# Optimization experiments

Hardware: AMD Instinct MI355X
Metric: run time of the kernel (lower is better)

The kernel has to match this reference:

```python
import jax, jax.numpy as jnp
import numpy as np

# Poincare ball hyperbolic multi-head attention (hypll-style HMultiheadAttention)
C = 1.0          # ball curvature
SQRT_C = 1.0
EPS = 1e-7
B, S, E, H = 4, 1024, 512, 8
HD = E // H      # head_dim = 64


def _project_to_ball(u, scale=0.5):
    n = jnp.linalg.norm(u, axis=-1, keepdims=True)
    return u * (scale / (1.0 + n))  # guarantees ||x|| < scale < 1/sqrt(C)


def h_linear(x, z, r):
    """Poincare fully-connected layer (Shimizu et al. HNN++), as in hypll HLinear.
    x: [..., n] points in the ball, z: [n, m] weight directions, r: [m] bias."""
    x2 = jnp.sum(x * x, -1, keepdims=True)
    lam = 2.0 / jnp.maximum(1.0 - C * x2, EPS)          # conformal factor lambda_x
    zn = jnp.maximum(jnp.linalg.norm(z, axis=0), EPS)    # [m]
    xz = x @ z                                           # [..., m]
    two_cr = 2.0 * SQRT_C * r
    v = (2.0 * zn / SQRT_C) * jnp.arcsinh(
        SQRT_C * lam * xz / zn * jnp.cosh(two_cr) - (lam - 1.0) * jnp.sinh(two_cr)
    )
    v2 = jnp.sum(v * v, -1, keepdims=True)
    return v / (1.0 + jnp.sqrt(1.0 + C * v2))            # map back into the ball


def _split_heads(x):
    b, s, e = x.shape
    return x.reshape(b, s, H, HD).transpose(0, 2, 1, 3)  # [B,H,S,hd]; matches split(dim=-1)


def _h_attention(q, k, v):
    # similarity = -poincare_dist(q, k), pairwise via the arccosh closed form
    # (avoids materializing a [B,H,Sq,Sk,hd] mobius_add tensor)
    q2 = jnp.sum(q * q, -1)[..., :, None]                # [B,H,Sq,1]
    k2 = jnp.sum(k * k, -1)[..., None, :]                # [B,H,1,Sk]
    qk = jnp.einsum('bhqd,bhkd->bhqk', q, k)
    diff2 = jnp.maximum(q2 + k2 - 2.0 * qk, 0.0)
    denom = jnp.maximum((1.0 - C * q2) * (1.0 - C * k2), EPS)
    arg = 1.0 + 2.0 * C * diff2 / denom
    dist = jnp.arccosh(jnp.maximum(arg, 1.0 + EPS)) / SQRT_C
    w = jax.nn.softmax(-dist, axis=-1)                   # attention_activation
    # attention_midpoint: weighted Mobius gyromidpoint then half scalar-mul
    v2 = jnp.sum(v * v, -1)                              # [B,H,Sk]
    lam = 2.0 / jnp.maximum(1.0 - C * v2, EPS)
    num = jnp.einsum('bhqk,bhkd->bhqd', w * lam[..., None, :], v)
    den = jnp.einsum('bhqk,bhk->bhq', w, lam - 1.0)[..., None]
    m_bar = num / jnp.where(jnp.abs(den) < EPS, EPS, den)
    mn = jnp.maximum(jnp.linalg.norm(m_bar, axis=-1, keepdims=True), EPS)
    t = jnp.minimum(SQRT_C * mn, 1.0 - 1e-6)
    return jnp.tanh(0.5 * jnp.arctanh(t)) * m_bar / (SQRT_C * mn)  # (1/2) mobius-scalar-mul


def setup_inputs() -> dict:
    key = jax.random.key(0)
    ks = jax.random.split(key, 9)
    query = _project_to_ball(jax.random.normal(ks[0], (B, S, E), jnp.float32))
    key_t = _project_to_ball(jax.random.normal(ks[1], (B, S, E), jnp.float32))
    value = _project_to_ball(jax.random.normal(ks[2], (B, S, E), jnp.float32))
    scale = E ** -0.5
    zq = jax.random.normal(ks[3], (E, E), jnp.float32) * scale
    zk = jax.random.normal(ks[4], (E, E), jnp.float32) * scale
    zv = jax.random.normal(ks[5], (E, E), jnp.float32) * scale
    rq = jax.random.normal(ks[6], (E,), jnp.float32) * 0.01
    rk = jax.random.normal(ks[7], (E,), jnp.float32) * 0.01
    rv = jax.random.normal(ks[8], (E,), jnp.float32) * 0.01
    return {"query": query, "key": key_t, "value": value,
            "zq": zq, "rq": rq, "zk": zk, "rk": rk, "zv": zv, "rv": rv}


def reference(query, key, value, zq, rq, zk, rk, zv, rv):
    pq = h_linear(query, zq, rq)
    pk = h_linear(key, zk, rk)
    pv = h_linear(value, zv, rv)
    q, k, v = _split_heads(pq), _split_heads(pk), _split_heads(pv)
    out = _h_attention(q, k, v)                          # [B,H,S,hd]
    return out.transpose(0, 2, 1, 3).reshape(B, S, E)    # manifold.cat over heads
```

## Files before the change

kernel.cpp:

```cpp
#include <hip/hip_runtime.h>
#include <hip/hip_bf16.h>
#include <math.h>

#define EPSf 1e-7f
typedef unsigned short u16;
typedef __attribute__((ext_vector_type(8))) short bf16x8;
typedef __attribute__((ext_vector_type(4))) float f32x4;

__device__ __forceinline__ float bf2f(u16 u) {
  union { unsigned int i; float f; } x; x.i = ((unsigned int)u) << 16; return x.f;
}
__device__ __forceinline__ u16 f2bf(float f) {
  union { float f; unsigned int i; } x; x.f = f;
  unsigned int r = x.i + 0x7fffu + ((x.i >> 16) & 1u);
  return (u16)(r >> 16);
}
__device__ __forceinline__ void gll16(const void* g, void* l) {
  __builtin_amdgcn_global_load_lds((__attribute__((address_space(1))) void*)(g),
                                   (__attribute__((address_space(3))) void*)(l),
                                   16, 0, 0);
}

__global__ __launch_bounds__(256) void split_x(
    const float* __restrict__ xq, const float* __restrict__ xk, const float* __restrict__ xv,
    u16* __restrict__ Xh, u16* __restrict__ Xl,
    float* __restrict__ Xn, float* __restrict__ Vn, float* __restrict__ Zn) {
  if (blockIdx.x == 0) {
    #pragma unroll
    for (int j = 0; j < 6; ++j) Zn[threadIdx.x + 256 * j] = 0.f;
  }
  const int gr = blockIdx.x * 2 + (threadIdx.x >> 7);
  const int mat = gr >> 12, row = gr & 4095;
  const float* X = (mat == 0) ? xq : (mat == 1) ? xk : xv;
  const int f4 = threadIdx.x & 127;
  float4 x = ((const float4*)(X + (size_t)row * 512))[f4];
  u16 h0 = f2bf(x.x), h1 = f2bf(x.y), h2 = f2bf(x.z), h3 = f2bf(x.w);
  u16 l0 = f2bf(x.x - bf2f(h0)), l1 = f2bf(x.y - bf2f(h1));
  u16 l2 = f2bf(x.z - bf2f(h2)), l3 = f2bf(x.w - bf2f(h3));
  ((ushort4*)(Xh + (size_t)gr * 512))[f4] = make_ushort4(h0, h1, h2, h3);
  ((ushort4*)(Xl + (size_t)gr * 512))[f4] = make_ushort4(l0, l1, l2, l3);
  float a = fmaf(x.x, x.x, fmaf(x.y, x.y, fmaf(x.z, x.z, x.w * x.w)));
  a += __shfl_xor(a, 1);  a += __shfl_xor(a, 2);  a += __shfl_xor(a, 4);
  a += __shfl_xor(a, 8);  a += __shfl_xor(a, 16); a += __shfl_xor(a, 32);
  __shared__ float red[4];
  if ((threadIdx.x & 63) == 0) red[threadIdx.x >> 6] = a;
  __syncthreads();
  if (threadIdx.x == 0)   { Xn[gr] = red[0] + red[1]; Vn[gr] = 0.f; }
  if (threadIdx.x == 128) { Xn[gr] = red[2] + red[3]; Vn[gr] = 0.f; }
}

__global__ __launch_bounds__(256) void split_z(
    const float* __restrict__ zq, const float* __restrict__ zk, const float* __restrict__ zv,
    u16* __restrict__ ZhT, u16* __restrict__ ZlT, float* __restrict__ Zn) {
  const int idx = blockIdx.x;
  const int mat = idx >> 6;
  const int cg = (idx >> 3) & 7, kt = idx & 7;
  const int c0 = cg * 64;
  const float* Z = (mat == 0) ? zq : (mat == 1) ? zk : zv;
  __shared__ float tile[64][68];
  const int t = threadIdx.x;
  {
    int kl = t >> 2;
    const float* src = Z + (size_t)(kt * 64 + kl) * 512 + c0 + (t & 3) * 16;
    #pragma unroll
    for (int j = 0; j < 4; ++j) {
      float4 v = *(const float4*)(src + 4 * j);
      *(float4*)&tile[kl][(t & 3) * 16 + 4 * j] = v;
    }
  }
  __syncthreads();
  const int cl = t >> 2, kg4 = t & 3;
  const size_t zo = (size_t)mat * 512 * 512;
  float csum = 0.f;
  #pragma unroll
  for (int jj = 0; jj < 4; ++jj) {
    u16 hb[4], lb[4];
    #pragma unroll
    for (int qq = 0; qq < 4; ++qq) {
      float zval = tile[kg4 * 16 + jj * 4 + qq][cl];
      csum = fmaf(zval, zval, csum);
      u16 hh = f2bf(zval);
      hb[qq] = hh;
      lb[qq] = f2bf(zval - bf2f(hh));
    }
    size_t o = zo + (size_t)(c0 + cl) * 512 + kt * 64 + kg4 * 16 + jj * 4;
    *(ushort4*)(ZhT + o) = make_ushort4(hb[0], hb[1], hb[2], hb[3]);
    *(ushort4*)(ZlT + o) = make_ushort4(lb[0], lb[1], lb[2], lb[3]);
  }
  csum += __shfl_xor(csum, 1);
  csum += __shfl_xor(csum, 2);
  if (kg4 == 0) atomicAdd(&Zn[mat * 512 + c0 + cl], csum);
}

__global__ __launch_bounds__(256) void proj_gemm(
    const u16* __restrict__ Xh, const u16* __restrict__ Xl,
    const u16* __restrict__ ZhT, const u16* __restrict__ ZlT,
    const float* __restrict__ Xn, const float* __restrict__ Zn,
    const float* __restrict__ rq, const float* __restrict__ rk, const float* __restrict__ rv,
    float* __restrict__ Vtmp, float* __restrict__ Vn) {
  const int m0 = blockIdx.x * 64;
  const int n0 = blockIdx.y * 128;
  const int mat = blockIdx.z;
  const size_t xoff = (size_t)mat * 4096 * 512;
  const size_t zoff = (size_t)mat * 512 * 512;
  const int t = threadIdx.x, wv = t >> 6, lane = t & 63;
  const int l15 = lane & 15, quad = lane >> 4;
  const int wm = wv >> 1, wn = wv & 1;

  __shared__ __align__(16) u16 SM[12288];
  __shared__ float lams[64], lam1s[64], wmxs[128], wmys[128], wmzs[128];

  if (t < 64) {
    float x2 = Xn[mat * 4096 + m0 + t];
    float lam = 2.f / fmaxf(1.f - x2, EPSf);
    lams[t] = lam; lam1s[t] = lam - 1.f;
  }
  if (t < 128) {
    float zn = fmaxf(sqrtf(Zn[mat * 512 + n0 + t]), EPSf);
    const float* R = (mat == 0) ? rq : (mat == 1) ? rk : rv;
    float tr = 2.f * R[n0 + t];
    float e = expf(tr), ei = 1.f / e;
    wmxs[t] = 0.5f * (e + ei) / zn;
    wmys[t] = 0.5f * (e - ei);
    wmzs[t] = 2.f * zn;
  }

  f32x4 acc[2][4];
  #pragma unroll
  for (int i = 0; i < 2; ++i)
    #pragma unroll
    for (int j = 0; j < 4; ++j) acc[i][j] = (f32x4){0.f, 0.f, 0.f, 0.f};

  const u16* gs[6];
  u16* ld[6];
  #pragma unroll
  for (int ci = 0; ci < 6; ++ci) {
    int c = wv + 4 * ci;
    const u16* arr; int row0, lo;
    if (c < 4)       { arr = Xh + xoff;  row0 = m0 + 16 * c;        lo = c * 512; }
    else if (c < 8)  { arr = Xl + xoff;  row0 = m0 + 16 * (c - 4);  lo = 2048 + (c - 4) * 512; }
    else if (c < 16) { arr = ZhT + zoff; row0 = n0 + 16 * (c - 8);  lo = 4096 + (c - 8) * 512; }
    else             { arr = ZlT + zoff; row0 = n0 + 16 * (c - 16); lo = 8192 + (c - 16) * 512; }
    gs[ci] = arr + (size_t)(row0 + (lane >> 2)) * 512 + (lane & 3) * 8;
    ld[ci] = SM + lo;
  }

  for (int k0 = 0; k0 < 512; k0 += 32) {
    __syncthreads();
    #pragma unroll
    for (int ci = 0; ci < 6; ++ci) gll16(gs[ci] + k0, ld[ci]);
    __syncthreads();
    bf16x8 ah[2], al[2], bh_[4], bl_[4];
    #pragma unroll
    for (int i = 0; i < 2; ++i) {
      int ra = wm * 32 + i * 16 + l15;
      ah[i] = *(const bf16x8*)&SM[ra * 32 + quad * 8];
      al[i] = *(const bf16x8*)&SM[2048 + ra * 32 + quad * 8];
    }
    #pragma unroll
    for (int j = 0; j < 4; ++j) {
      int rb = wn * 64 + j * 16 + l15;
      bh_[j] = *(const bf16x8*)&SM[4096 + rb * 32 + quad * 8];
      bl_[j] = *(const bf16x8*)&SM[8192 + rb * 32 + quad * 8];
    }
    #pragma unroll
    for (int i = 0; i < 2; ++i)
      #pragma unroll
      for (int j = 0; j < 4; ++j) {
        acc[i][j] = __builtin_amdgcn_mfma_f32_16x16x32_bf16(ah[i], bh_[j], acc[i][j], 0, 0, 0);
        acc[i][j] = __builtin_amdgcn_mfma_f32_16x16x32_bf16(ah[i], bl_[j], acc[i][j], 0, 0, 0);
        acc[i][j] = __builtin_amdgcn_mfma_f32_16x16x32_bf16(al[i], bh_[j], acc[i][j], 0, 0, 0);
      }
  }

  #pragma unroll
  for (int i = 0; i < 2; ++i) {
    float rsum[4] = {0.f, 0.f, 0.f, 0.f};
    #pragma unroll
    for (int j = 0; j < 4; ++j) {
      int nl = wn * 64 + j * 16 + l15;
      float wx = wmxs[nl], wy = wmys[nl], wz = wmzs[nl];
      #pragma unroll
      for (int r = 0; r < 4; ++r) {
        int ml = wm * 32 + i * 16 + quad * 4 + r;
        float tt = lams[ml] * acc[i][j][r] * wx - lam1s[ml] * wy;
        float v = wz * logf(tt + sqrtf(fmaf(tt, tt, 1.f)));
        Vtmp[xoff + (size_t)(m0 + ml) * 512 + (n0 + nl)] = v;
        rsum[r] = fmaf(v, v, rsum[r]);
      }
    }
    #pragma unroll
    for (int r = 0; r < 4; ++r) {
      rsum[r] += __shfl_xor(rsum[r], 1);
      rsum[r] += __shfl_xor(rsum[r], 2);
      rsum[r] += __shfl_xor(rsum[r], 4);
      rsum[r] += __shfl_xor(rsum[r], 8);
    }
    if (l15 == 0) {
      #pragma unroll
      for (int r = 0; r < 4; ++r)
        atomicAdd(&Vn[mat * 4096 + m0 + wm * 32 + i * 16 + quad * 4 + r], rsum[r]);
    }
  }
}

__global__ __launch_bounds__(256) void pack(
    const float* __restrict__ Vtmp, const float* __restrict__ Vn,
    u16* __restrict__ Qh, u16* __restrict__ Kh, u16* __restrict__ VTb,
    float* __restrict__ q2a, float* __restrict__ aqa, float4* __restrict__ ksc) {
  __shared__ u16 tile[64][72];
  __shared__ float lams[64];
  const int t = threadIdx.x;
  if (blockIdx.x < 256) {
    const int mat = blockIdx.x >> 7;
    const int rb = blockIdx.x & 127;
    const int r = t >> 3, h = t & 7;
    const int row = rb * 32 + r;
    const size_t gr = (size_t)mat * 4096 + row;
    const float sc = 1.f / (1.f + sqrtf(1.f + Vn[gr]));
    const float* src = Vtmp + gr * 512 + h * 64;
    const int b = row >> 10, s = row & 1023;
    u16* dst = (mat ? Kh : Qh) + ((size_t)(b * 8 + h) * 1024 + s) * 64;
    float nrm = 0.f;
    #pragma unroll
    for (int j = 0; j < 16; ++j) {
      float4 x = *(const float4*)(src + 4 * j);
      u16 u0 = f2bf(x.x * sc), u1 = f2bf(x.y * sc), u2 = f2bf(x.z * sc), u3 = f2bf(x.w * sc);
      *(ushort4*)(dst + 4 * j) = make_ushort4(u0, u1, u2, u3);
      float f0 = bf2f(u0), f1 = bf2f(u1), f2 = bf2f(u2), f3 = bf2f(u3);
      nrm += f0 * f0 + f1 * f1 + f2 * f2 + f3 * f3;
    }
    const size_t so = (size_t)(b * 8 + h) * 1024 + s;
    if (mat == 0) { q2a[so] = nrm; aqa[so] = 1.f / fmaxf(1.f - nrm, EPSf); }
    else {
      float2 kk = make_float2(nrm, 2.f / fmaxf(1.f - nrm, EPSf));
      *(float2*)&ksc[so] = kk;
    }
  } else {
    const int idx = blockIdx.x - 256;
    const int bh = idx >> 4, st = idx & 15;
    const int b = bh >> 3, h = bh & 7;
    {
      const int s = t >> 2, dg = t & 3;
      const size_t gr = (size_t)2 * 4096 + b * 1024 + st * 64 + s;
      const float sc = 1.f / (1.f + sqrtf(1.f + Vn[gr]));
      const float* src = Vtmp + gr * 512 + h * 64 + dg * 16;
      float nrm = 0.f;
      #pragma unroll
      for (int j = 0; j < 4; ++j) {
        float4 x = *(const float4*)(src + 4 * j);
        u16 u0 = f2bf(x.x * sc), u1 = f2bf(x.y * sc), u2 = f2bf(x.z * sc), u3 = f2bf(x.w * sc);
        *(ushort4*)&tile[s][dg * 16 + 4 * j] = make_ushort4(u0, u1, u2, u3);
        float f0 = bf2f(u0), f1 = bf2f(u1), f2 = bf2f(u2), f3 = bf2f(u3);
        nrm += f0 * f0 + f1 * f1 + f2 * f2 + f3 * f3;
      }
      nrm += __shfl_xor(nrm, 1);
      nrm += __shfl_xor(nrm, 2);
      if (dg == 0) {
        float lam = 2.f / fmaxf(1.f - nrm, EPSf);
        lams[s] = lam;
        ((float*)&ksc[(size_t)bh * 1024 + st * 64 + s])[3] = lam - 1.f;
      }
    }
    __syncthreads();
    const int d = t >> 2, sg = t & 3;
    u16 ob[16];
    #pragma unroll
    for (int j = 0; j < 16; ++j) {
      int ss = sg * 16 + j;
      ob[j] = f2bf(bf2f(tile[ss][d]) * lams[ss]);
    }
    u16* dst = VTb + ((size_t)bh * 64 + d) * 1024 + st * 64 + sg * 16;
    #pragma unroll
    for (int j = 0; j < 4; ++j)
      *(ushort4*)(dst + 4 * j) = make_ushort4(ob[4 * j], ob[4 * j + 1], ob[4 * j + 2], ob[4 * j + 3]);
  }
}

__global__ __launch_bounds__(256, 2) void attn(
    const u16* __restrict__ Qh, const u16* __restrict__ Kh, const u16* __restrict__ VTb,
    const float* __restrict__ q2a, const float* __restrict__ aqa,
    const float4* __restrict__ ksc, float* __restrict__ out) {
  const int bh = blockIdx.x;
  const int b = bh >> 3, h = bh & 7;
  const int q0 = blockIdx.y * 64;
  const int t = threadIdx.x, wv = t >> 6, lane = t & 63;
  const int l15 = lane & 15, quad = lane >> 4;
  const int qh = wv & 1, kh = wv >> 1;

  __shared__ __align__(16) u16 Ws[4][32 * 72];
  __shared__ float k2s[4][64], cks[4][64], l1s[4][64];
  __shared__ __align__(16) float nums[2][32][68];
  __shared__ float dens[2][32];

  const size_t qkoff = (size_t)bh * 65536;

  bf16x8 qf[2][2];
  float q2r[2], aqr[2];
  #pragma unroll
  for (int qs = 0; qs < 2; ++qs) {
    int qrow = q0 + qh * 32 + qs * 16 + l15;
    const u16* qp = Qh + qkoff + (size_t)qrow * 64 + quad * 8;
    qf[qs][0] = *(const bf16x8*)qp;
    qf[qs][1] = *(const bf16x8*)(qp + 32);
    q2r[qs] = q2a[bh * 1024 + qrow];
    aqr[qs] = aqa[bh * 1024 + qrow];
  }

  f32x4 num[2][4];
  #pragma unroll
  for (int qs = 0; qs < 2; ++qs)
    #pragma unroll
    for (int tm = 0; tm < 4; ++tm) num[qs][tm] = (f32x4){0.f, 0.f, 0.f, 0.f};
  float denp[2] = {0.f, 0.f};

  bf16x8 kcur[8];
  #pragma unroll
  for (int tn = 0; tn < 4; ++tn)
    #pragma unroll
    for (int ks = 0; ks < 2; ++ks)
      kcur[tn * 2 + ks] = *(const bf16x8*)(Kh + qkoff +
          (size_t)(kh * 64 + tn * 16 + l15) * 64 + ks * 32 + quad * 8);
  float4 scur = ksc[bh * 1024 + kh * 64 + lane];

  #pragma unroll 2
  for (int i = 0; i < 8; ++i) {
    const int ktc = kh + 2 * i;
    const int kti = (i < 7) ? ktc + 2 : ktc;
    bf16x8 knxt[8];
    #pragma unroll
    for (int tn = 0; tn < 4; ++tn)
      #pragma unroll
      for (int ks = 0; ks < 2; ++ks)
        knxt[tn * 2 + ks] = *(const bf16x8*)(Kh + qkoff +
            (size_t)(kti * 64 + tn * 16 + l15) * 64 + ks * 32 + quad * 8);
    float4 snxt = ksc[bh * 1024 + kti * 64 + lane];
    bf16x8 vf[8];
    #pragma unroll
    for (int tm = 0; tm < 4; ++tm)
      #pragma unroll
      for (int ks = 0; ks < 2; ++ks)
        vf[tm * 2 + ks] = *(const bf16x8*)(VTb + qkoff +
            (size_t)(tm * 16 + l15) * 1024 + ktc * 64 + ks * 32 + quad * 8);
    k2s[wv][lane] = scur.x;
    cks[wv][lane] = scur.y;
    l1s[wv][lane] = scur.w;

    #pragma unroll
    for (int tn = 0; tn < 4; ++tn) {
      const float4 k2v = *(const float4*)&k2s[wv][tn * 16 + quad * 4];
      const float4 ckv = *(const float4*)&cks[wv][tn * 16 + quad * 4];
      const float4 l1v = *(const float4*)&l1s[wv][tn * 16 + quad * 4];
      #pragma unroll
      for (int qs = 0; qs < 2; ++qs) {
        f32x4 s = (f32x4){0.f, 0.f, 0.f, 0.f};
        s = __builtin_amdgcn_mfma_f32_16x16x32_bf16(kcur[tn * 2 + 0], qf[qs][0], s, 0, 0, 0);
        s = __builtin_amdgcn_mfma_f32_16x16x32_bf16(kcur[tn * 2 + 1], qf[qs][1], s, 0, 0, 0);
        unsigned up[2];
        #pragma unroll
        for (int pr = 0; pr < 2; ++pr) {
          float w2[2];
          #pragma unroll
          for (int e = 0; e < 2; ++e) {
            const int r = pr * 2 + e;
            float d2 = fmaxf(fmaf(-2.f, s[r], q2r[qs] + ((const float*)&k2v)[r]), 0.f);
            float u = fmaxf(d2 * ((const float*)&ckv)[r] * aqr[qs], EPSf);
            w2[e] = (1.f + u) - sqrtf(fmaf(u, u, u + u));
          }
          union { __hip_bfloat162 h2; unsigned u; } cv;
          cv.h2 = __float22bfloat162_rn(make_float2(w2[0], w2[1]));
          up[pr] = cv.u;
          float wlo = __uint_as_float(cv.u << 16);
          float whi = __uint_as_float(cv.u & 0xffff0000u);
          denp[qs] = fmaf(wlo, ((const float*)&l1v)[pr * 2 + 0], denp[qs]);
          denp[qs] = fmaf(whi, ((const float*)&l1v)[pr * 2 + 1], denp[qs]);
        }
        *(uint2*)&Ws[wv][(qs * 16 + l15) * 72 + tn * 16 + quad * 4] = make_uint2(up[0], up[1]);
      }
    }
    #pragma unroll
    for (int qs = 0; qs < 2; ++qs)
      #pragma unroll
      for (int ks = 0; ks < 2; ++ks) {
        const bf16x8 wf = *(const bf16x8*)&Ws[wv][(qs * 16 + l15) * 72 + ks * 32 + quad * 8];
        #pragma unroll
        for (int tm = 0; tm < 4; ++tm)
          num[qs][tm] = __builtin_amdgcn_mfma_f32_16x16x32_bf16(vf[tm * 2 + ks], wf, num[qs][tm], 0, 0, 0);
      }
    #pragma unroll
    for (int j = 0; j < 8; ++j) kcur[j] = knxt[j];
    scur = snxt;
  }

  #pragma unroll
  for (int qs = 0; qs < 2; ++qs) {
    denp[qs] += __shfl_xor(denp[qs], 16);
    denp[qs] += __shfl_xor(denp[qs], 32);
  }
  if (kh == 1) {
    #pragma unroll
    for (int qs = 0; qs < 2; ++qs) {
      #pragma unroll
      for (int tm = 0; tm < 4; ++tm)
        *(float4*)&nums[qh][qs * 16 + l15][tm * 16 + quad * 4] =
            make_float4(num[qs][tm][0], num[qs][tm][1], num[qs][tm][2], num[qs][tm][3]);
      if (quad == 0) dens[qh][qs * 16 + l15] = denp[qs];
    }
  }
  __syncthreads();
  if (kh == 0) {
    #pragma unroll
    for (int qs = 0; qs < 2; ++qs) {
      float den = denp[qs] + dens[qh][qs * 16 + l15];
      den = (fabsf(den) < EPSf) ? EPSf : den;
      float inv = 1.f / den;
      float mv[4][4];
      float p = 0.f;
      #pragma unroll
      for (int tm = 0; tm < 4; ++tm) {
        float4 o = *(const float4*)&nums[qh][qs * 16 + l15][tm * 16 + quad * 4];
        mv[tm][0] = (num[qs][tm][0] + o.x) * inv;
        mv[tm][1] = (num[qs][tm][1] + o.y) * inv;
        mv[tm][2] = (num[qs][tm][2] + o.z) * inv;
        mv[tm][3] = (num[qs][tm][3] + o.w) * inv;
        p = fmaf(mv[tm][0], mv[tm][0], p); p = fmaf(mv[tm][1], mv[tm][1], p);
        p = fmaf(mv[tm][2], mv[tm][2], p); p = fmaf(mv[tm][3], mv[tm][3], p);
      }
      p += __shfl_xor(p, 16);
      p += __shfl_xor(p, 32);
      float mn = sqrtf(p);
      float mnc = fmaxf(mn, EPSf);
      float tt2 = fminf(mnc, 1.f - 1e-6f);
      float scale = tt2 / ((1.f + sqrtf(fmaxf(1.f - tt2 * tt2, 0.f))) * mnc);
      const size_t qg = (size_t)b * 1024 + q0 + qh * 32 + qs * 16 + l15;
      #pragma unroll
      for (int tm = 0; tm < 4; ++tm) {
        float4 o = make_float4(mv[tm][0] * scale, mv[tm][1] * scale,
                               mv[tm][2] * scale, mv[tm][3] * scale);
        *(float4*)(out + qg * 512 + h * 64 + tm * 16 + quad * 4) = o;
      }
    }
  }
}

extern "C" void kernel_launch(void* const* d_in, const int* in_sizes, int n_in,
                              void* d_out, int out_size, void* d_ws, size_t ws_size,
                              hipStream_t stream) {
  (void)in_sizes; (void)n_in; (void)out_size; (void)ws_size;
  const float* q  = (const float*)d_in[0];
  const float* k  = (const float*)d_in[1];
  const float* v  = (const float*)d_in[2];
  const float* zq = (const float*)d_in[3];
  const float* rq = (const float*)d_in[4];
  const float* zk = (const float*)d_in[5];
  const float* rk = (const float*)d_in[6];
  const float* zv = (const float*)d_in[7];
  const float* rv = (const float*)d_in[8];

  unsigned char* ws = (unsigned char*)d_ws;
  u16*   Xh   = (u16*)(ws + 0);
  u16*   Xl   = (u16*)(ws + 12582912);
  u16*   ZhT  = (u16*)(ws + 25165824);
  u16*   ZlT  = (u16*)(ws + 26738688);
  float* Vtmp = (float*)(ws + 28311552);
  float* Xn   = (float*)(ws + 53477376);
  float* Vn   = (float*)(ws + 53526528);
  float* Zn   = (float*)(ws + 53575680);
  u16*   Qh   = (u16*)(ws + 0);
  u16*   Kh   = (u16*)(ws + 4194304);
  u16*   VTb  = (u16*)(ws + 8388608);
  float* q2a  = (float*)(ws + 12582912);
  float* aqa  = (float*)(ws + 12713984);
  float4* ksc = (float4*)(ws + 12845056);

  split_x<<<6144, 256, 0, stream>>>(q, k, v, Xh, Xl, Xn, Vn, Zn);
  split_z<<<192, 256, 0, stream>>>(zq, zk, zv, ZhT, ZlT, Zn);
  proj_gemm<<<dim3(64, 4, 3), 256, 0, stream>>>(Xh, Xl, ZhT, ZlT, Xn, Zn, rq, rk, rv, Vtmp, Vn);
  pack<<<768, 256, 0, stream>>>(Vtmp, Vn, Qh, Kh, VTb, q2a, aqa, ksc);
  attn<<<dim3(32, 16), 256, 0, stream>>>(Qh, Kh, VTb, q2a, aqa, ksc, (float*)d_out);
}
```

Baseline: 177.3 us.

## Software-pipeline the PV MFMA one iteration behind the QK score stage

The attention loop is restructured so the weighted-value MFMA for key tile i-1 runs in iteration i, using weights read back from LDS and a V fragment loaded during the previous iteration. The separate knxt double buffer is removed: the next K tile is loaded straight into kcur after the score computation, and a final PV step after the loop drains the pipeline. The goal is to overlap V and K global loads with the score and PV math while lowering register pressure. The trade-off is a shorter prefetch distance for K, which is now issued later in each iteration, so its latency may be less well hidden.

New measurement: 174.0 us. No clear change (-1.8%).

```diff
diff --git a/kernel.cpp b/kernel.cpp
--- a/kernel.cpp
+++ b/kernel.cpp
@@ -323,25 +323,22 @@
           (size_t)(kh * 64 + tn * 16 + l15) * 64 + ks * 32 + quad * 8);
   float4 scur = ksc[bh * 1024 + kh * 64 + lane];
 
+  bf16x8 vfp[8];
+  #pragma unroll
+  for (int j = 0; j < 8; ++j) vfp[j] = (bf16x8){0,0,0,0,0,0,0,0};
+
   #pragma unroll 2
   for (int i = 0; i < 8; ++i) {
     const int ktc = kh + 2 * i;
     const int kti = (i < 7) ? ktc + 2 : ktc;
-    bf16x8 knxt[8];
-    #pragma unroll
-    for (int tn = 0; tn < 4; ++tn)
+
+    bf16x8 wfp[2][2];
+    #pragma unroll
+    for (int qs = 0; qs < 2; ++qs)
       #pragma unroll
       for (int ks = 0; ks < 2; ++ks)
-        knxt[tn * 2 + ks] = *(const bf16x8*)(Kh + qkoff +
-            (size_t)(kti * 64 + tn * 16 + l15) * 64 + ks * 32 + quad * 8);
-    float4 snxt = ksc[bh * 1024 + kti * 64 + lane];
-    bf16x8 vf[8];
-    #pragma unroll
-    for (int tm = 0; tm < 4; ++tm)
-      #pragma unroll
-      for (int ks = 0; ks < 2; ++ks)
-        vf[tm * 2 + ks] = *(const bf16x8*)(VTb + qkoff +
-            (size_t)(tm * 16 + l15) * 1024 + ktc * 64 + ks * 32 + quad * 8);
+        wfp[qs][ks] = *(const bf16x8*)&Ws[wv][(qs * 16 + l15) * 72 + ks * 32 + quad * 8];
+
     k2s[wv][lane] = scur.x;
     cks[wv][lane] = scur.y;
     l1s[wv][lane] = scur.w;
@@ -378,6 +375,37 @@
         *(uint2*)&Ws[wv][(qs * 16 + l15) * 72 + tn * 16 + quad * 4] = make_uint2(up[0], up[1]);
       }
     }
+
+    #pragma unroll
+    for (int tn = 0; tn < 4; ++tn)
+      #pragma unroll
+      for (int ks = 0; ks < 2; ++ks)
+        kcur[tn * 2 + ks] = *(const bf16x8*)(Kh + qkoff +
+            (size_t)(kti * 64 + tn * 16 + l15) * 64 + ks * 32 + quad * 8);
+    float4 snxt = ksc[bh * 1024 + kti * 64 + lane];
+
+    if (i) {
+      #pragma unroll
+      for (int qs = 0; qs < 2; ++qs)
+        #pragma unroll
+        for (int ks = 0; ks < 2; ++ks)
+          #pragma unroll
+          for (int tm = 0; tm < 4; ++tm)
+            num[qs][tm] = __builtin_amdgcn_mfma_f32_16x16x32_bf16(
+                vfp[tm * 2 + ks], wfp[qs][ks], num[qs][tm], 0, 0, 0);
+    }
+
+    #pragma unroll
+    for (int tm = 0; tm < 4; ++tm)
+      #pragma unroll
+      for (int ks = 0; ks < 2; ++ks)
+        vfp[tm * 2 + ks] = *(const bf16x8*)(VTb + qkoff +
+            (size_t)(tm * 16 + l15) * 1024 + ktc * 64 + ks * 32 + quad * 8);
+
+    scur = snxt;
+  }
+
+  {
     #pragma unroll
     for (int qs = 0; qs < 2; ++qs)
       #pragma unroll
@@ -385,11 +413,9 @@
         const bf16x8 wf = *(const bf16x8*)&Ws[wv][(qs * 16 + l15) * 72 + ks * 32 + quad * 8];
         #pragma unroll
         for (int tm = 0; tm < 4; ++tm)
-          num[qs][tm] = __builtin_amdgcn_mfma_f32_16x16x32_bf16(vf[tm * 2 + ks], wf, num[qs][tm], 0, 0, 0);
-      }
-    #pragma unroll
-    for (int j = 0; j < 8; ++j) kcur[j] = knxt[j];
-    scur = snxt;
+          num[qs][tm] = __builtin_amdgcn_mfma_f32_16x16x32_bf16(
+              vfp[tm * 2 + ks], wf, num[qs][tm], 0, 0, 0);
+      }
   }
 
   #pragma unroll
```

## Split attention keys across four waves and load GEMM B operands directly

Applied to the files above, without the earlier changes.

In the attention kernel, each block now covers 32 queries instead of 64, with each of the four waves handling a quarter of the keys. A two-level LDS tree reduction then combines the partial numerators and denominators. The grid doubles and launch bounds allow 4 blocks per CU, aiming for more parallelism and occupancy at the cost of loading K/V twice as often. The projection GEMM also stops staging the weight (B) tiles in LDS and reads them straight from global memory into registers, which shrinks LDS but may lower reuse and coalescing.

New measurement: 233.7 us. 1.32x slower.

```diff
diff --git a/kernel.cpp b/kernel.cpp
--- a/kernel.cpp
+++ b/kernel.cpp
@@ -107,7 +107,7 @@
   const int l15 = lane & 15, quad = lane >> 4;
   const int wm = wv >> 1, wn = wv & 1;
 
-  __shared__ __align__(16) u16 SM[12288];
+  __shared__ __align__(16) u16 SM[4096];
   __shared__ float lams[64], lam1s[64], wmxs[128], wmys[128], wmzs[128];
 
   if (t < 64) {
@@ -116,7 +116,7 @@
     lams[t] = lam; lam1s[t] = lam - 1.f;
   }
   if (t < 128) {
-    float zn = fmaxf(sqrtf(Zn[mat * 512 + n0 + t]), EPSf);
+    float zn = fmaxf(sqrtf(Zn[mat * 512 + t + n0]), EPSf);
     const float* R = (mat == 0) ? rq : (mat == 1) ? rk : rv;
     float tr = 2.f * R[n0 + t];
     float e = expf(tr), ei = 1.f / e;
@@ -131,37 +131,37 @@
     #pragma unroll
     for (int j = 0; j < 4; ++j) acc[i][j] = (f32x4){0.f, 0.f, 0.f, 0.f};
 
-  const u16* gs[6];
-  u16* ld[6];
-  #pragma unroll
-  for (int ci = 0; ci < 6; ++ci) {
+  const u16* gs[2];
+  u16* ld[2];
+  #pragma unroll
+  for (int ci = 0; ci < 2; ++ci) {
     int c = wv + 4 * ci;
     const u16* arr; int row0, lo;
-    if (c < 4)       { arr = Xh + xoff;  row0 = m0 + 16 * c;        lo = c * 512; }
-    else if (c < 8)  { arr = Xl + xoff;  row0 = m0 + 16 * (c - 4);  lo = 2048 + (c - 4) * 512; }
-    else if (c < 16) { arr = ZhT + zoff; row0 = n0 + 16 * (c - 8);  lo = 4096 + (c - 8) * 512; }
-    else             { arr = ZlT + zoff; row0 = n0 + 16 * (c - 16); lo = 8192 + (c - 16) * 512; }
+    if (c < 4) { arr = Xh + xoff; row0 = m0 + 16 * c;       lo = c * 512; }
+    else       { arr = Xl + xoff; row0 = m0 + 16 * (c - 4); lo = 2048 + (c - 4) * 512; }
     gs[ci] = arr + (size_t)(row0 + (lane >> 2)) * 512 + (lane & 3) * 8;
     ld[ci] = SM + lo;
   }
+  const u16* gBh = ZhT + zoff + (size_t)(n0 + wn * 64 + l15) * 512 + quad * 8;
+  const u16* gBl = ZlT + zoff + (size_t)(n0 + wn * 64 + l15) * 512 + quad * 8;
 
   for (int k0 = 0; k0 < 512; k0 += 32) {
     __syncthreads();
-    #pragma unroll
-    for (int ci = 0; ci < 6; ++ci) gll16(gs[ci] + k0, ld[ci]);
+    gll16(gs[0] + k0, ld[0]);
+    gll16(gs[1] + k0, ld[1]);
+    bf16x8 bh_[4], bl_[4];
+    #pragma unroll
+    for (int j = 0; j < 4; ++j) {
+      bh_[j] = *(const bf16x8*)(gBh + (size_t)(j * 16) * 512 + k0);
+      bl_[j] = *(const bf16x8*)(gBl + (size_t)(j * 16) * 512 + k0);
+    }
     __syncthreads();
-    bf16x8 ah[2], al[2], bh_[4], bl_[4];
+    bf16x8 ah[2], al[2];
     #pragma unroll
     for (int i = 0; i < 2; ++i) {
       int ra = wm * 32 + i * 16 + l15;
       ah[i] = *(const bf16x8*)&SM[ra * 32 + quad * 8];
       al[i] = *(const bf16x8*)&SM[2048 + ra * 32 + quad * 8];
-    }
-    #pragma unroll
-    for (int j = 0; j < 4; ++j) {
-      int rb = wn * 64 + j * 16 + l15;
-      bh_[j] = *(const bf16x8*)&SM[4096 + rb * 32 + quad * 8];
-      bl_[j] = *(const bf16x8*)&SM[8192 + rb * 32 + quad * 8];
     }
     #pragma unroll
     for (int i = 0; i < 2; ++i)
@@ -277,16 +277,16 @@
   }
 }
 
-__global__ __launch_bounds__(256, 2) void attn(
+__global__ __launch_bounds__(256, 4) void attn(
     const u16* __restrict__ Qh, const u16* __restrict__ Kh, const u16* __restrict__ VTb,
     const float* __restrict__ q2a, const float* __restrict__ aqa,
     const float4* __restrict__ ksc, float* __restrict__ out) {
   const int bh = blockIdx.x;
   const int b = bh >> 3, h = bh & 7;
-  const int q0 = blockIdx.y * 64;
+  const int q0 = blockIdx.y * 32;
   const int t = threadIdx.x, wv = t >> 6, lane = t & 63;
   const int l15 = lane & 15, quad = lane >> 4;
-  const int qh = wv & 1, kh = wv >> 1;
+  const int kq = wv;
 
   __shared__ __align__(16) u16 Ws[4][32 * 72];
   __shared__ float k2s[4][64], cks[4][64], l1s[4][64];
@@ -299,7 +299,7 @@
   float q2r[2], aqr[2];
   #pragma unroll
   for (int qs = 0; qs < 2; ++qs) {
-    int qrow = q0 + qh * 32 + qs * 16 + l15;
+    int qrow = q0 + qs * 16 + l15;
     const u16* qp = Qh + qkoff + (size_t)qrow * 64 + quad * 8;
     qf[qs][0] = *(const bf16x8*)qp;
     qf[qs][1] = *(const bf16x8*)(qp + 32);
@@ -320,13 +320,13 @@
     #pragma unroll
     for (int ks = 0; ks < 2; ++ks)
       kcur[tn * 2 + ks] = *(const bf16x8*)(Kh + qkoff +
-          (size_t)(kh * 64 + tn * 16 + l15) * 64 + ks * 32 + quad * 8);
-  float4 scur = ksc[bh * 1024 + kh * 64 + lane];
+          (size_t)(kq * 64 + tn * 16 + l15) * 64 + ks * 32 + quad * 8);
+  float4 scur = ksc[bh * 1024 + kq * 64 + lane];
 
   #pragma unroll 2
-  for (int i = 0; i < 8; ++i) {
-    const int ktc = kh + 2 * i;
-    const int kti = (i < 7) ? ktc + 2 : ktc;
+  for (int i = 0; i < 4; ++i) {
+    const int ktc = kq + 4 * i;
+    const int kti = (i < 3) ? ktc + 4 : ktc;
     bf16x8 knxt[8];
     #pragma unroll
     for (int tn = 0; tn < 4; ++tn)
@@ -385,7 +385,8 @@
         const bf16x8 wf = *(const bf16x8*)&Ws[wv][(qs * 16 + l15) * 72 + ks * 32 + quad * 8];
         #pragma unroll
         for (int tm = 0; tm < 4; ++tm)
-          num[qs][tm] = __builtin_amdgcn_mfma_f32_16x16x32_bf16(vf[tm * 2 + ks], wf, num[qs][tm], 0, 0, 0);
+          num[qs][tm] = __builtin_amdgcn_mfma_f32_16x16x32_bf16(
+              vf[tm * 2 + ks], wf, num[qs][tm], 0, 0, 0);
       }
     #pragma unroll
     for (int j = 0; j < 8; ++j) kcur[j] = knxt[j];
@@ -397,32 +398,63 @@
     denp[qs] += __shfl_xor(denp[qs], 16);
     denp[qs] += __shfl_xor(denp[qs], 32);
   }
-  if (kh == 1) {
+
+  if (wv & 1) {
+    const int buf = wv >> 1;
     #pragma unroll
     for (int qs = 0; qs < 2; ++qs) {
       #pragma unroll
       for (int tm = 0; tm < 4; ++tm)
-        *(float4*)&nums[qh][qs * 16 + l15][tm * 16 + quad * 4] =
+        *(float4*)&nums[buf][qs * 16 + l15][tm * 16 + quad * 4] =
             make_float4(num[qs][tm][0], num[qs][tm][1], num[qs][tm][2], num[qs][tm][3]);
-      if (quad == 0) dens[qh][qs * 16 + l15] = denp[qs];
+      if (quad == 0) dens[buf][qs * 16 + l15] = denp[qs];
     }
   }
   __syncthreads();
-  if (kh == 0) {
+  if (!(wv & 1)) {
+    const int buf = wv >> 1;
     #pragma unroll
     for (int qs = 0; qs < 2; ++qs) {
-      float den = denp[qs] + dens[qh][qs * 16 + l15];
+      #pragma unroll
+      for (int tm = 0; tm < 4; ++tm) {
+        float4 o = *(const float4*)&nums[buf][qs * 16 + l15][tm * 16 + quad * 4];
+        num[qs][tm][0] += o.x; num[qs][tm][1] += o.y;
+        num[qs][tm][2] += o.z; num[qs][tm][3] += o.w;
+      }
+      denp[qs] += dens[buf][qs * 16 + l15];
+    }
+  }
+  if (wv == 2) {
+    #pragma unroll
+    for (int qs = 0; qs < 2; ++qs) {
+      #pragma unroll
+      for (int tm = 0; tm < 4; ++tm)
+        *(float4*)&nums[1][qs * 16 + l15][tm * 16 + quad * 4] =
+            make_float4(num[qs][tm][0], num[qs][tm][1], num[qs][tm][2], num[qs][tm][3]);
+      if (quad == 0) dens[1][qs * 16 + l15] = denp[qs];
+    }
+  }
+  __syncthreads();
+  if (wv == 0) {
+    #pragma unroll
+    for (int qs = 0; qs < 2; ++qs) {
+      #pragma unroll
+      for (int tm = 0; tm < 4; ++tm) {
+        float4 o = *(const float4*)&nums[1][qs * 16 + l15][tm * 16 + quad * 4];
+        num[qs][tm][0] += o.x; num[qs][tm][1] += o.y;
+        num[qs][tm][2] += o.z; num[qs][tm][3] += o.w;
+      }
+      float den = denp[qs] + dens[1][qs * 16 + l15];
       den = (fabsf(den) < EPSf) ? EPSf : den;
       float inv = 1.f / den;
       float mv[4][4];
       float p = 0.f;
       #pragma unroll
       for (int tm = 0; tm < 4; ++tm) {
-        float4 o = *(const float4*)&nums[qh][qs * 16 + l15][tm * 16 + quad * 4];
-        mv[tm][0] = (num[qs][tm][0] + o.x) * inv;
-        mv[tm][1] = (num[qs][tm][1] + o.y) * inv;
-        mv[tm][2] = (num[qs][tm][2] + o.z) * inv;
-        mv[tm][3] = (num[qs][tm][3] + o.w) * inv;
+        mv[tm][0] = num[qs][tm][0] * inv;
+        mv[tm][1] = num[qs][tm][1] * inv;
+        mv[tm][2] = num[qs][tm][2] * inv;
+        mv[tm][3] = num[qs][tm][3] * inv;
         p = fmaf(mv[tm][0], mv[tm][0], p); p = fmaf(mv[tm][1], mv[tm][1], p);
         p = fmaf(mv[tm][2], mv[tm][2], p); p = fmaf(mv[tm][3], mv[tm][3], p);
       }
@@ -432,7 +464,7 @@
       float mnc = fmaxf(mn, EPSf);
       float tt2 = fminf(mnc, 1.f - 1e-6f);
       float scale = tt2 / ((1.f + sqrtf(fmaxf(1.f - tt2 * tt2, 0.f))) * mnc);
-      const size_t qg = (size_t)b * 1024 + q0 + qh * 32 + qs * 16 + l15;
+      const size_t qg = (size_t)b * 1024 + q0 + qs * 16 + l15;
       #pragma unroll
       for (int tm = 0; tm < 4; ++tm) {
         float4 o = make_float4(mv[tm][0] * scale, mv[tm][1] * scale,
@@ -477,5 +509,5 @@
   split_z<<<192, 256, 0, stream>>>(zq, zk, zv, ZhT, ZlT, Zn);
   proj_gemm<<<dim3(64, 4, 3), 256, 0, stream>>>(Xh, Xl, ZhT, ZlT, Xn, Zn, rq, rk, rv, Vtmp, Vn);
   pack<<<768, 256, 0, stream>>>(Vtmp, Vn, Qh, Kh, VTb, q2a, aqa, ksc);
-  attn<<<dim3(32, 16), 256, 0, stream>>>(Qh, Kh, VTb, q2a, aqa, ksc, (float*)d_out);
-}
+  attn<<<dim3(32, 32), 256, 0, stream>>>(Qh, Kh, VTb, q2a, aqa, ksc, (float*)d_out);
+}
```
